# Kernel tuning notes

Hardware: AMD Instinct MI355X
Metric: run time of the kernel (lower is better)

## Reference

```python
import jax, jax.numpy as jnp
import numpy as np

N_USERS = 52643
N_ITEMS = 91599
N = N_USERS + N_ITEMS  # 144242 nodes
M_PAIRS = 1_000_000    # user-item interactions -> 2M symmetric directed edges
D = 64


def setup_inputs() -> dict:
    key = jax.random.key(0)
    k1, k2, k3, k4, k5 = jax.random.split(key, 5)
    # bipartite interactions, symmetrized: A = [[0, R], [R^T, 0]]
    u = jax.random.randint(k1, (M_PAIRS,), 0, N_USERS, dtype=jnp.int32)
    it = jax.random.randint(k2, (M_PAIRS,), N_USERS, N, dtype=jnp.int32)
    row = jnp.concatenate([u, it])
    col = jnp.concatenate([it, u])
    embed = jax.random.normal(k3, (N, D), dtype=jnp.float32)
    W1 = jax.random.normal(k4, (D, D), dtype=jnp.float32) * 0.01  # linear.weight
    W2 = jax.random.normal(k5, (D, D), dtype=jnp.float32) * 0.01  # interActTransform.weight
    b1 = jnp.zeros((D,), jnp.float32)
    b2 = jnp.zeros((D,), jnp.float32)
    return {"embed": embed, "row": row, "col": col,
            "W1": W1, "b1": b1, "W2": W2, "b2": b2}


def reference(embed, row, col, W1, b1, W2, b2):
    n = embed.shape[0]
    # degree of symmetric A (row sums), D^-1/2 normalization
    deg = jax.ops.segment_sum(jnp.ones(row.shape, embed.dtype), row, num_segments=n)
    dinv = jnp.where(deg > 0, jax.lax.rsqrt(jnp.maximum(deg, 1.0)), 0.0)
    vals = dinv[row] * dinv[col]  # L = D^-1/2 A D^-1/2 (COO values)

    def spmm(x):  # [n, d] -> L @ x
        return jax.ops.segment_sum(vals[:, None] * x[col], row, num_segments=n)

    h1 = embed + spmm(embed)        # L1 @ embed, L1 = L + I
    h2 = spmm(embed * embed)        # L2 @ embed^2
    # nn.Linear: x @ W^T + b
    return (h1 @ W1.T + b1) + (h2 @ W2.T + b2)
```

## Files before the change

kernel.cpp:

```cpp
#include <hip/hip_runtime.h>


#define NB 256
#define MAXBUCK 608
#define RECCAP 8192

typedef short bf16x8 __attribute__((ext_vector_type(8)));
typedef float f32x4 __attribute__((ext_vector_type(4)));

__device__ __forceinline__ float bf2f(unsigned short u) {
    union { unsigned int i; float f; } c; c.i = ((unsigned int)u) << 16; return c.f;
}
__device__ __forceinline__ unsigned int f2bf(float f) {
    union { float f; unsigned int i; } c; c.f = f;
    unsigned int r = c.i + 0x7FFFu + ((c.i >> 16) & 1u);
    return r >> 16;
}
__device__ __forceinline__ unsigned int pk2(float a, float b) {
    return f2bf(a) | (f2bf(b) << 16);
}


__global__ __launch_bounds__(256) void k1_count(const int* __restrict__ row,
                                                const int* __restrict__ col,
                                                int* __restrict__ H, int Eh, int nbuck) {
    __shared__ int hist[MAXBUCK];
    int tid = threadIdx.x, b = blockIdx.x;
    for (int i = tid; i < nbuck; i += 256) hist[i] = 0;
    __syncthreads();
    int chunk = (Eh + NB - 1) / NB;
    int e0 = b * chunk, e1 = min(e0 + chunk, Eh);
    for (int e = e0 + tid; e < e1; e += 256) {
        int u = row[e], v = col[e];
        atomicAdd(&hist[u >> 8], 1);
        atomicAdd(&hist[v >> 8], 1);
    }
    __syncthreads();
    for (int i = tid; i < nbuck; i += 256) H[b * nbuck + i] = hist[i];
}

__global__ __launch_bounds__(256) void k2_colscan(const int* __restrict__ H,
                                                  int* __restrict__ Off,
                                                  int* __restrict__ btot, int nbuck) {
    __shared__ int lds[256];
    int t = threadIdx.x, beta = blockIdx.x;
    int v = H[t * nbuck + beta];
    lds[t] = v;
    __syncthreads();
    for (int off = 1; off < 256; off <<= 1) {
        int x = (t >= off) ? lds[t - off] : 0;
        __syncthreads();
        lds[t] += x;
        __syncthreads();
    }
    Off[beta * NB + t] = lds[t] - v;
    if (t == 255) btot[beta] = lds[255];
}

__global__ __launch_bounds__(1024) void k2b_bscan(const int* __restrict__ btot,
                                                  int* __restrict__ bbase, int nbuck,
                                                  int E, int* __restrict__ start, int n) {
    __shared__ int lds[1024];
    int t = threadIdx.x;
    int v = (t < nbuck) ? btot[t] : 0;
    lds[t] = v;
    __syncthreads();
    for (int off = 1; off < 1024; off <<= 1) {
        int x = (t >= off) ? lds[t - off] : 0;
        __syncthreads();
        lds[t] += x;
        __syncthreads();
    }
    if (t < nbuck) bbase[t] = lds[t] - v;
    if (t == nbuck) bbase[t] = E;
    if (t == 0) start[n] = E;
}

__global__ __launch_bounds__(256) void k3_scatter(const int* __restrict__ row,
                                                  const int* __restrict__ col,
                                                  const int* __restrict__ Off,
                                                  const int* __restrict__ bbase,
                                                  unsigned int* __restrict__ rec,
                                                  int Eh, int nbuck) {
    __shared__ int cur[MAXBUCK];
    int tid = threadIdx.x, b = blockIdx.x;
    for (int i = tid; i < nbuck; i += 256) cur[i] = bbase[i] + Off[i * NB + b];
    __syncthreads();
    int chunk = (Eh + NB - 1) / NB;
    int e0 = b * chunk, e1 = min(e0 + chunk, Eh);
    for (int e = e0 + tid; e < e1; e += 256) {
        int u = row[e], v = col[e];
        int p = atomicAdd(&cur[u >> 8], 1);
        rec[p] = ((unsigned int)v << 8) | (u & 255);
        int q = atomicAdd(&cur[v >> 8], 1);
        rec[q] = ((unsigned int)u << 8) | (v & 255);
    }
}

__global__ __launch_bounds__(256) void k4_local(const unsigned int* __restrict__ rec,
                                                const int* __restrict__ bbase,
                                                int* __restrict__ start,
                                                float* __restrict__ dinv,
                                                int* __restrict__ scol, int n) {
    __shared__ int hist[256], lcur[256], lds[256];
    __shared__ unsigned int cache[RECCAP];
    int t = threadIdx.x, beta = blockIdx.x;
    int base = bbase[beta];
    int cnt = bbase[beta + 1] - base;
    bool cached = cnt <= RECCAP;
    hist[t] = 0;
    __syncthreads();
    for (int r = t; r < cnt; r += 256) {
        unsigned int rr = rec[base + r];
        if (cached) cache[r] = rr;
        atomicAdd(&hist[rr & 255], 1);
    }
    __syncthreads();
    int h = hist[t];
    lds[t] = h;
    __syncthreads();
    for (int off = 1; off < 256; off <<= 1) {
        int x = (t >= off) ? lds[t - off] : 0;
        __syncthreads();
        lds[t] += x;
        __syncthreads();
    }
    int excl = lds[t] - h;
    int node = (beta << 8) + t;
    if (node < n) {
        start[node] = base + excl;
        dinv[node] = h > 0 ? rsqrtf((float)h) : 0.0f;
    }
    lcur[t] = base + excl;
    __syncthreads();
    for (int r = t; r < cnt; r += 256) {
        unsigned int rr = cached ? cache[r] : rec[base + r];
        int p = atomicAdd(&lcur[rr & 255], 1);
        scol[p] = (int)(rr >> 8);
    }
}

__global__ __launch_bounds__(256) void k_xform(
    const float4* __restrict__ embed4, const float* __restrict__ dinv,
    const float4* __restrict__ W1_4, const float4* __restrict__ W2_4,
    const float* __restrict__ b1, const float* __restrict__ b2,
    unsigned int* __restrict__ y1p, unsigned int* __restrict__ zp, int n) {
    __shared__ __align__(16) unsigned int lW[2][2048];
    __shared__ __align__(16) unsigned int lA[4][2][512];

    int tid = threadIdx.x;
    int wave = tid >> 6, lane = tid & 63;
    int L = lane & 15, hi = lane >> 4;

#pragma unroll
    for (int p = 0; p < 8; p++) {
        int idx = p * 256 + tid;
        int mat = idx >> 10, rem = idx & 1023;
        int row = rem >> 4, col4 = rem & 15;
        float4 v = (mat ? W2_4 : W1_4)[rem];
        int dw = (row * 32 + col4 * 2) ^ ((row & 7) << 2);
        *(int2*)&lW[mat][dw] = make_int2(pk2(v.x, v.y), pk2(v.z, v.w));
    }
    __syncthreads();

    bf16x8 bfr[2][4][2];
#pragma unroll
    for (int m = 0; m < 2; m++)
#pragma unroll
        for (int t = 0; t < 4; t++)
#pragma unroll
            for (int kf = 0; kf < 2; kf++) {
                int row = 16 * t + L;
                int dw = (row * 32 + kf * 16 + hi * 4) ^ ((L & 7) << 2);
                int4 raw = *(const int4*)&lW[m][dw];
                bfr[m][t][kf] = *(bf16x8*)&raw;
            }

    int tb16 = blockIdx.x * 64 + wave * 16;
#pragma unroll
    for (int p = 0; p < 4; p++) {
        int idx = p * 64 + lane;
        int row = idx >> 4, col4 = idx & 15;
        int node = tb16 + row;
        int nc = node < n ? node : n - 1;
        float4 v = embed4[(size_t)nc * 16 + col4];
        int dw = (row * 32 + col4 * 2) ^ ((row & 7) << 2);
        *(int2*)&lA[wave][0][dw] = make_int2(pk2(v.x, v.y), pk2(v.z, v.w));
        *(int2*)&lA[wave][1][dw] = make_int2(pk2(v.x * v.x, v.y * v.y),
                                             pk2(v.z * v.z, v.w * v.w));
    }

    f32x4 accY[4], accS[4];
#pragma unroll
    for (int t = 0; t < 4; t++) { accY[t] = (f32x4)0.f; accS[t] = (f32x4)0.f; }
#pragma unroll
    for (int kf = 0; kf < 2; kf++) {
        int dw = (L * 32 + kf * 16 + hi * 4) ^ ((L & 7) << 2);
        int4 rawE = *(const int4*)&lA[wave][0][dw];
        int4 rawQ = *(const int4*)&lA[wave][1][dw];
        bf16x8 aE = *(bf16x8*)&rawE;
        bf16x8 aQ = *(bf16x8*)&rawQ;
#pragma unroll
        for (int t = 0; t < 4; t++) {
            accY[t] = __builtin_amdgcn_mfma_f32_16x16x32_bf16(aE, bfr[0][t][kf], accY[t], 0, 0, 0);
            accS[t] = __builtin_amdgcn_mfma_f32_16x16x32_bf16(aQ, bfr[1][t][kf], accS[t], 0, 0, 0);
        }
    }

    float bs0 = b1[L] + b2[L];
    float bs1 = b1[16 + L] + b2[16 + L];
    float bs2 = b1[32 + L] + b2[32 + L];
    float bs3 = b1[48 + L] + b2[48 + L];
#pragma unroll
    for (int r = 0; r < 4; r++) {
        int node = tb16 + 4 * hi + r;
        if (node >= n) continue;
        float di = dinv[node];
        float y0 = accY[0][r], y1 = accY[1][r], y2 = accY[2][r], y3 = accY[3][r];
        float s0 = accS[0][r], s1 = accS[1][r], s2 = accS[2][r], s3 = accS[3][r];
        size_t base = (size_t)node * 32;
        y1p[base + L]      = pk2(y0 + bs0, y2 + bs2);
        y1p[base + 16 + L] = pk2(y1 + bs1, y3 + bs3);
        zp[base + L]       = pk2(di * (y0 + s0), di * (y2 + s2));
        zp[base + 16 + L]  = pk2(di * (y1 + s1), di * (y3 + s3));
    }
}

__global__ __launch_bounds__(256, 8) void k_main(
    const ushort4* __restrict__ zb4, const ushort4* __restrict__ y1b4,
    const int* __restrict__ start, const int* __restrict__ scol,
    const float* __restrict__ dinv, float2* __restrict__ out2, int n) {
    int tid = threadIdx.x;
    int wave = tid >> 6, lane = tid & 63, g = lane >> 4, l = lane & 15;
    int i = blockIdx.x * 16 + wave * 4 + g;
    bool valid = i < n;
    int ii = valid ? i : 0;
    int s0 = start[ii];
    int s1 = valid ? start[ii + 1] : s0;

    float4 acc = make_float4(0.f, 0.f, 0.f, 0.f);
    for (int e = s0; e < s1; e += 16) {
        int cnt = s1 - e;
        cnt = cnt > 16 ? 16 : cnt;
        int jv = scol[e + (l < cnt ? l : 0)];
#pragma unroll 8
        for (int k = 0; k < 16; k++) {
            int j = __shfl(jv, (g << 4) + k, 64);
            float m = (k < cnt) ? 1.0f : 0.0f;
            ushort4 z = zb4[(size_t)j * 16 + l];
            acc.x = fmaf(bf2f(z.x), m, acc.x);
            acc.y = fmaf(bf2f(z.y), m, acc.y);
            acc.z = fmaf(bf2f(z.z), m, acc.z);
            acc.w = fmaf(bf2f(z.w), m, acc.w);
        }
    }
    if (valid) {
        float di = dinv[i];
        ushort4 yb = y1b4[(size_t)i * 16 + l];
        float4 o;
        o.x = fmaf(di, acc.x, bf2f(yb.x));
        o.y = fmaf(di, acc.y, bf2f(yb.y));
        o.z = fmaf(di, acc.z, bf2f(yb.z));
        o.w = fmaf(di, acc.w, bf2f(yb.w));
        out2[(size_t)i * 32 + l] = make_float2(o.x, o.z);
        out2[(size_t)i * 32 + 16 + l] = make_float2(o.y, o.w);
    }
}

extern "C" void kernel_launch(void* const* d_in, const int* in_sizes, int n_in,
                              void* d_out, int out_size, void* d_ws, size_t ws_size,
                              hipStream_t stream) {
    const float* embed = (const float*)d_in[0];
    const int* row = (const int*)d_in[1];
    const int* col = (const int*)d_in[2];
    const float* W1 = (const float*)d_in[3];
    const float* b1 = (const float*)d_in[4];
    const float* W2 = (const float*)d_in[5];
    const float* b2 = (const float*)d_in[6];
    float* out = (float*)d_out;

    int n = in_sizes[0] / 64;
    int E = in_sizes[1];
    int Eh = E / 2;
    int nbuck = (n + 255) >> 8;
    size_t n64 = (size_t)n * 64;
    if (nbuck > MAXBUCK) return;
    if (n >= (1 << 18)) return;

    char* ws = (char*)d_ws;
    size_t off = 0;
    unsigned int* zp = (unsigned int*)(ws + off);  off += n64 * 2;
    unsigned int* y1p = (unsigned int*)(ws + off); off += n64 * 2;
    unsigned int* rec = (unsigned int*)(ws + off); off += (size_t)E * 4;
    int* scol = (int*)(ws + off);                  off += (size_t)E * 4;
    int* H = (int*)(ws + off);                     off += (size_t)NB * nbuck * 4;
    int* Off = (int*)(ws + off);                   off += (size_t)nbuck * NB * 4;
    int* btot = (int*)(ws + off);                  off += (size_t)nbuck * 4;
    int* bbase = (int*)(ws + off);                 off += (size_t)(nbuck + 1) * 4;
    int* start = (int*)(ws + off);                 off += (size_t)(n + 1) * 4;
    float* dinv = (float*)(ws + off);              off += (size_t)n * 4;

    if (off > ws_size) return;

    k1_count<<<NB, 256, 0, stream>>>(row, col, H, Eh, nbuck);
    k2_colscan<<<nbuck, 256, 0, stream>>>(H, Off, btot, nbuck);
    k2b_bscan<<<1, 1024, 0, stream>>>(btot, bbase, nbuck, E, start, n);
    k3_scatter<<<NB, 256, 0, stream>>>(row, col, Off, bbase, rec, Eh, nbuck);
    k4_local<<<nbuck, 256, 0, stream>>>(rec, bbase, start, dinv, scol, n);
    k_xform<<<(n + 63) / 64, 256, 0, stream>>>((const float4*)embed, dinv,
                                               (const float4*)W1, (const float4*)W2,
                                               b1, b2, y1p, zp, n);
    k_main<<<(n + 15) / 16, 256, 0, stream>>>((const ushort4*)zp, (const ushort4*)y1p,
                                              start, scol, dinv, (float2*)out, n);
}
```

Measured before the change: 103.2 us.

## Drop bucket-scan kernel via atomic allocation, vectorize edge loads, nontemporal memory ops

Removes the single-block bucket scan kernel. Bucket bases are now assigned with a global atomicAdd in the column-scan kernel, and per-node end offsets are stored explicitly, so buckets no longer need to be contiguous in order. The count and scatter kernels load row and col as int4 to cut load instructions. The SpMM kernel reads bf16 pairs as 32-bit words and uses nontemporal loads and stores for the streaming arrays. This saves one launch, but the rec/scol layout now depends on atomic ordering and becomes nondeterministic across runs.

Result: slower. 106.8 us (+3.5%).

```diff
diff --git a/kernel.cpp b/kernel.cpp
--- a/kernel.cpp
+++ b/kernel.cpp
@@ -7,9 +7,17 @@
 
 typedef short bf16x8 __attribute__((ext_vector_type(8)));
 typedef float f32x4 __attribute__((ext_vector_type(4)));
+typedef float f32x2 __attribute__((ext_vector_type(2)));
+typedef unsigned int u32x2 __attribute__((ext_vector_type(2)));
 
 __device__ __forceinline__ float bf2f(unsigned short u) {
     union { unsigned int i; float f; } c; c.i = ((unsigned int)u) << 16; return c.f;
+}
+__device__ __forceinline__ float bflo(unsigned int u) {
+    union { unsigned int i; float f; } c; c.i = u << 16; return c.f;
+}
+__device__ __forceinline__ float bfhi(unsigned int u) {
+    union { unsigned int i; float f; } c; c.i = u & 0xffff0000u; return c.f;
 }
 __device__ __forceinline__ unsigned int f2bf(float f) {
     union { float f; unsigned int i; } c; c.f = f;
@@ -23,17 +31,32 @@
 
 __global__ __launch_bounds__(256) void k1_count(const int* __restrict__ row,
                                                 const int* __restrict__ col,
-                                                int* __restrict__ H, int Eh, int nbuck) {
+                                                int* __restrict__ H,
+                                                int* __restrict__ galloc,
+                                                int Eh, int nbuck) {
     __shared__ int hist[MAXBUCK];
     int tid = threadIdx.x, b = blockIdx.x;
+    if (b == 0 && tid == 0) *galloc = 0;
     for (int i = tid; i < nbuck; i += 256) hist[i] = 0;
     __syncthreads();
-    int chunk = (Eh + NB - 1) / NB;
-    int e0 = b * chunk, e1 = min(e0 + chunk, Eh);
-    for (int e = e0 + tid; e < e1; e += 256) {
-        int u = row[e], v = col[e];
-        atomicAdd(&hist[u >> 8], 1);
-        atomicAdd(&hist[v >> 8], 1);
+    int chunk = (((Eh + NB - 1) / NB) + 3) & ~3;
+    int e0 = b * chunk;
+    int len = Eh - e0;
+    if (len > chunk) len = chunk;
+    if (len < 0) len = 0;
+    int len4 = len & ~3;
+    for (int o = tid * 4; o < len4; o += 1024) {
+        int4 u = *(const int4*)&row[e0 + o];
+        int4 v = *(const int4*)&col[e0 + o];
+        atomicAdd(&hist[u.x >> 8], 1); atomicAdd(&hist[v.x >> 8], 1);
+        atomicAdd(&hist[u.y >> 8], 1); atomicAdd(&hist[v.y >> 8], 1);
+        atomicAdd(&hist[u.z >> 8], 1); atomicAdd(&hist[v.z >> 8], 1);
+        atomicAdd(&hist[u.w >> 8], 1); atomicAdd(&hist[v.w >> 8], 1);
+    }
+    if (tid < len - len4) {
+        int e = e0 + len4 + tid;
+        atomicAdd(&hist[row[e] >> 8], 1);
+        atomicAdd(&hist[col[e] >> 8], 1);
     }
     __syncthreads();
     for (int i = tid; i < nbuck; i += 256) H[b * nbuck + i] = hist[i];
@@ -41,7 +64,9 @@
 
 __global__ __launch_bounds__(256) void k2_colscan(const int* __restrict__ H,
                                                   int* __restrict__ Off,
-                                                  int* __restrict__ btot, int nbuck) {
+                                                  int* __restrict__ btot,
+                                                  int* __restrict__ bbase,
+                                                  int* __restrict__ galloc, int nbuck) {
     __shared__ int lds[256];
     int t = threadIdx.x, beta = blockIdx.x;
     int v = H[t * nbuck + beta];
@@ -54,26 +79,11 @@
         __syncthreads();
     }
     Off[beta * NB + t] = lds[t] - v;
-    if (t == 255) btot[beta] = lds[255];
-}
-
-__global__ __launch_bounds__(1024) void k2b_bscan(const int* __restrict__ btot,
-                                                  int* __restrict__ bbase, int nbuck,
-                                                  int E, int* __restrict__ start, int n) {
-    __shared__ int lds[1024];
-    int t = threadIdx.x;
-    int v = (t < nbuck) ? btot[t] : 0;
-    lds[t] = v;
-    __syncthreads();
-    for (int off = 1; off < 1024; off <<= 1) {
-        int x = (t >= off) ? lds[t - off] : 0;
-        __syncthreads();
-        lds[t] += x;
-        __syncthreads();
-    }
-    if (t < nbuck) bbase[t] = lds[t] - v;
-    if (t == nbuck) bbase[t] = E;
-    if (t == 0) start[n] = E;
+    if (t == 255) {
+        int tot = lds[255];
+        btot[beta] = tot;
+        bbase[beta] = atomicAdd(galloc, tot);
+    }
 }
 
 __global__ __launch_bounds__(256) void k3_scatter(const int* __restrict__ row,
@@ -86,9 +96,27 @@
     int tid = threadIdx.x, b = blockIdx.x;
     for (int i = tid; i < nbuck; i += 256) cur[i] = bbase[i] + Off[i * NB + b];
     __syncthreads();
-    int chunk = (Eh + NB - 1) / NB;
-    int e0 = b * chunk, e1 = min(e0 + chunk, Eh);
-    for (int e = e0 + tid; e < e1; e += 256) {
+    int chunk = (((Eh + NB - 1) / NB) + 3) & ~3;
+    int e0 = b * chunk;
+    int len = Eh - e0;
+    if (len > chunk) len = chunk;
+    if (len < 0) len = 0;
+    int len4 = len & ~3;
+    for (int o = tid * 4; o < len4; o += 1024) {
+        int4 u = *(const int4*)&row[e0 + o];
+        int4 v = *(const int4*)&col[e0 + o];
+        int p;
+        p = atomicAdd(&cur[u.x >> 8], 1); rec[p] = ((unsigned int)v.x << 8) | (u.x & 255);
+        p = atomicAdd(&cur[v.x >> 8], 1); rec[p] = ((unsigned int)u.x << 8) | (v.x & 255);
+        p = atomicAdd(&cur[u.y >> 8], 1); rec[p] = ((unsigned int)v.y << 8) | (u.y & 255);
+        p = atomicAdd(&cur[v.y >> 8], 1); rec[p] = ((unsigned int)u.y << 8) | (v.y & 255);
+        p = atomicAdd(&cur[u.z >> 8], 1); rec[p] = ((unsigned int)v.z << 8) | (u.z & 255);
+        p = atomicAdd(&cur[v.z >> 8], 1); rec[p] = ((unsigned int)u.z << 8) | (v.z & 255);
+        p = atomicAdd(&cur[u.w >> 8], 1); rec[p] = ((unsigned int)v.w << 8) | (u.w & 255);
+        p = atomicAdd(&cur[v.w >> 8], 1); rec[p] = ((unsigned int)u.w << 8) | (v.w & 255);
+    }
+    if (tid < len - len4) {
+        int e = e0 + len4 + tid;
         int u = row[e], v = col[e];
         int p = atomicAdd(&cur[u >> 8], 1);
         rec[p] = ((unsigned int)v << 8) | (u & 255);
@@ -99,14 +127,16 @@
 
 __global__ __launch_bounds__(256) void k4_local(const unsigned int* __restrict__ rec,
                                                 const int* __restrict__ bbase,
+                                                const int* __restrict__ btot,
                                                 int* __restrict__ start,
+                                                int* __restrict__ send,
                                                 float* __restrict__ dinv,
                                                 int* __restrict__ scol, int n) {
     __shared__ int hist[256], lcur[256], lds[256];
     __shared__ unsigned int cache[RECCAP];
     int t = threadIdx.x, beta = blockIdx.x;
     int base = bbase[beta];
-    int cnt = bbase[beta + 1] - base;
+    int cnt = btot[beta];
     bool cached = cnt <= RECCAP;
     hist[t] = 0;
     __syncthreads();
@@ -129,6 +159,7 @@
     int node = (beta << 8) + t;
     if (node < n) {
         start[node] = base + excl;
+        send[node] = base + excl + h;
         dinv[node] = h > 0 ? rsqrtf((float)h) : 0.0f;
     }
     lcur[t] = base + excl;
@@ -227,43 +258,46 @@
 }
 
 __global__ __launch_bounds__(256, 8) void k_main(
-    const ushort4* __restrict__ zb4, const ushort4* __restrict__ y1b4,
-    const int* __restrict__ start, const int* __restrict__ scol,
-    const float* __restrict__ dinv, float2* __restrict__ out2, int n) {
+    const unsigned int* __restrict__ zp, const unsigned int* __restrict__ y1p,
+    const int* __restrict__ start, const int* __restrict__ send,
+    const int* __restrict__ scol, const float* __restrict__ dinv,
+    f32x2* __restrict__ out2, int n) {
     int tid = threadIdx.x;
     int wave = tid >> 6, lane = tid & 63, g = lane >> 4, l = lane & 15;
     int i = blockIdx.x * 16 + wave * 4 + g;
     bool valid = i < n;
     int ii = valid ? i : 0;
     int s0 = start[ii];
-    int s1 = valid ? start[ii + 1] : s0;
+    int s1 = valid ? send[ii] : s0;
 
     float4 acc = make_float4(0.f, 0.f, 0.f, 0.f);
     for (int e = s0; e < s1; e += 16) {
         int cnt = s1 - e;
         cnt = cnt > 16 ? 16 : cnt;
-        int jv = scol[e + (l < cnt ? l : 0)];
+        int jv = __builtin_nontemporal_load(&scol[e + (l < cnt ? l : 0)]);
 #pragma unroll 8
         for (int k = 0; k < 16; k++) {
             int j = __shfl(jv, (g << 4) + k, 64);
             float m = (k < cnt) ? 1.0f : 0.0f;
-            ushort4 z = zb4[(size_t)j * 16 + l];
-            acc.x = fmaf(bf2f(z.x), m, acc.x);
-            acc.y = fmaf(bf2f(z.y), m, acc.y);
-            acc.z = fmaf(bf2f(z.z), m, acc.z);
-            acc.w = fmaf(bf2f(z.w), m, acc.w);
+            u32x2 zw = *(const u32x2*)&zp[(size_t)j * 32 + 2 * l];
+            acc.x = fmaf(bflo(zw[0]), m, acc.x);
+            acc.y = fmaf(bfhi(zw[0]), m, acc.y);
+            acc.z = fmaf(bflo(zw[1]), m, acc.z);
+            acc.w = fmaf(bfhi(zw[1]), m, acc.w);
         }
     }
     if (valid) {
         float di = dinv[i];
-        ushort4 yb = y1b4[(size_t)i * 16 + l];
+        u32x2 yw = __builtin_nontemporal_load((const u32x2*)&y1p[(size_t)i * 32 + 2 * l]);
         float4 o;
-        o.x = fmaf(di, acc.x, bf2f(yb.x));
-        o.y = fmaf(di, acc.y, bf2f(yb.y));
-        o.z = fmaf(di, acc.z, bf2f(yb.z));
-        o.w = fmaf(di, acc.w, bf2f(yb.w));
-        out2[(size_t)i * 32 + l] = make_float2(o.x, o.z);
-        out2[(size_t)i * 32 + 16 + l] = make_float2(o.y, o.w);
+        o.x = fmaf(di, acc.x, bflo(yw[0]));
+        o.y = fmaf(di, acc.y, bfhi(yw[0]));
+        o.z = fmaf(di, acc.z, bflo(yw[1]));
+        o.w = fmaf(di, acc.w, bfhi(yw[1]));
+        f32x2 lo2 = {o.x, o.z};
+        f32x2 hi2 = {o.y, o.w};
+        __builtin_nontemporal_store(lo2, &out2[(size_t)i * 32 + l]);
+        __builtin_nontemporal_store(hi2, &out2[(size_t)i * 32 + 16 + l]);
     }
 }
 
@@ -296,20 +330,21 @@
     int* H = (int*)(ws + off);                     off += (size_t)NB * nbuck * 4;
     int* Off = (int*)(ws + off);                   off += (size_t)nbuck * NB * 4;
     int* btot = (int*)(ws + off);                  off += (size_t)nbuck * 4;
-    int* bbase = (int*)(ws + off);                 off += (size_t)(nbuck + 1) * 4;
-    int* start = (int*)(ws + off);                 off += (size_t)(n + 1) * 4;
+    int* bbase = (int*)(ws + off);                 off += (size_t)nbuck * 4;
+    int* start = (int*)(ws + off);                 off += (size_t)n * 4;
+    int* send = (int*)(ws + off);                  off += (size_t)n * 4;
     float* dinv = (float*)(ws + off);              off += (size_t)n * 4;
+    int* galloc = (int*)(ws + off);                off += 64;
 
     if (off > ws_size) return;
 
-    k1_count<<<NB, 256, 0, stream>>>(row, col, H, Eh, nbuck);
-    k2_colscan<<<nbuck, 256, 0, stream>>>(H, Off, btot, nbuck);
-    k2b_bscan<<<1, 1024, 0, stream>>>(btot, bbase, nbuck, E, start, n);
+    k1_count<<<NB, 256, 0, stream>>>(row, col, H, galloc, Eh, nbuck);
+    k2_colscan<<<nbuck, 256, 0, stream>>>(H, Off, btot, bbase, galloc, nbuck);
     k3_scatter<<<NB, 256, 0, stream>>>(row, col, Off, bbase, rec, Eh, nbuck);
-    k4_local<<<nbuck, 256, 0, stream>>>(rec, bbase, start, dinv, scol, n);
+    k4_local<<<nbuck, 256, 0, stream>>>(rec, bbase, btot, start, send, dinv, scol, n);
     k_xform<<<(n + 63) / 64, 256, 0, stream>>>((const float4*)embed, dinv,
                                                (const float4*)W1, (const float4*)W2,
                                                b1, b2, y1p, zp, n);
-    k_main<<<(n + 15) / 16, 256, 0, stream>>>((const ushort4*)zp, (const ushort4*)y1p,
-                                              start, scol, dinv, (float2*)out, n);
-}
+    k_main<<<(n + 15) / 16, 256, 0, stream>>>(zp, y1p, start, send, scol, dinv,
+                                              (f32x2*)out, n);
+}
```
